# Optimization experiments

Hardware: AMD Instinct MI355X
Metric: run time of the kernel (lower is better)

The kernel has to match this reference:

```python
import jax, jax.numpy as jnp
import numpy as np

N = 100000
E = 1600000
IN_FEATS = 512
N_CLASSES = 40
H1, D1 = 8, 8
H2, D2 = 1, N_CLASSES


def gat_conv(x, src, dst, W, al, ar, b, H, D):
    # x: [N, F] -> h: [N, H, D]
    n = x.shape[0]
    h = (x @ W).reshape(n, H, D)
    el = (h * al[None]).sum(-1)  # [N, H]
    er = (h * ar[None]).sum(-1)  # [N, H]
    e = jax.nn.leaky_relu(el[src] + er[dst], 0.2)  # [E, H]
    # segment softmax over destination neighborhoods
    emax = jax.ops.segment_max(e, dst, num_segments=n)  # [N, H]
    ee = jnp.exp(e - emax[dst])
    denom = jax.ops.segment_sum(ee, dst, num_segments=n)  # [N, H]
    a = ee / (denom[dst] + 1e-9)  # [E, H]
    m = h[src] * a[:, :, None]  # [E, H, D]
    out = jax.ops.segment_sum(m, dst, num_segments=n)  # [N, H, D]
    return out + b.reshape(1, H, D)


def setup_inputs() -> dict:
    key = jax.random.key(0)
    ks = jax.random.split(key, 12)
    g1 = 1.0 / np.sqrt(IN_FEATS)
    g2 = 1.0 / np.sqrt(H1 * D1)
    return {
        "x": jax.random.normal(ks[0], (N, IN_FEATS), jnp.float32),
        "src": jax.random.randint(ks[1], (E,), 0, N, jnp.int32),
        "dst": jax.random.randint(ks[2], (E,), 0, N, jnp.int32),
        "W1": jax.random.normal(ks[3], (IN_FEATS, H1 * D1), jnp.float32) * g1,
        "al1": jax.random.normal(ks[4], (H1, D1), jnp.float32) * 0.1,
        "ar1": jax.random.normal(ks[5], (H1, D1), jnp.float32) * 0.1,
        "b1": jnp.zeros((H1 * D1,), jnp.float32),
        "W2": jax.random.normal(ks[6], (H1 * D1, H2 * D2), jnp.float32) * g2,
        "al2": jax.random.normal(ks[7], (H2, D2), jnp.float32) * 0.1,
        "ar2": jax.random.normal(ks[8], (H2, D2), jnp.float32) * 0.1,
        "b2": jnp.zeros((H2 * D2,), jnp.float32),
    }


def reference(x, src, dst, W1, al1, ar1, b1, W2, al2, ar2, b2):
    h = gat_conv(x, src, dst, W1, al1, ar1, b1, H1, D1)  # [N, 8, 8]
    h = jax.nn.elu(h.reshape(N, H1 * D1))  # [N, 64]
    h = gat_conv(h, src, dst, W2, al2, ar2, b2, H2, D2).mean(axis=1)  # [N, n_classes]
    return jax.nn.log_softmax(h, axis=1)
```

## Files before the change

### kernel.cpp

```cpp
#include <hip/hip_runtime.h>
#include <hip/hip_bf16.h>
#include <math.h>

#define NCLS 40
#define PWG 256
#define BSH 9
#define NBMAX 512
#define SRCB 23
#define CSRCAP 14336

typedef __attribute__((ext_vector_type(8))) short bf16x8;
typedef __attribute__((ext_vector_type(4))) float f32x4;

__device__ inline float bf2f(ushort u) {
    unsigned v = ((unsigned)u) << 16;
    float f;
    __builtin_memcpy(&f, &v, 4);
    return f;
}
__device__ inline ushort f2bf(float f) {
    unsigned v;
    __builtin_memcpy(&v, &f, 4);
    unsigned r = (v + 0x7FFFu + ((v >> 16) & 1u)) >> 16;
    return (ushort)r;
}

__global__ __launch_bounds__(256) void conv_prep_kernel(
    const float* __restrict__ W1, ushort* __restrict__ W1t,
    const float* __restrict__ W2, const float* __restrict__ al2,
    const float* __restrict__ ar2, float* __restrict__ wal2,
    float* __restrict__ war2)
{
    if (blockIdx.x < 128) {
        int id = blockIdx.x * 256 + threadIdx.x;
        int k = id >> 6, c = id & 63;
        W1t[c * 512 + k] = f2bf(W1[k * 64 + c]);
    } else {
        int k = threadIdx.x;
        if (k < 64) {
            float a = 0.f, b = 0.f;
            for (int c = 0; c < NCLS; c++) {
                float w = W2[k * NCLS + c];
                a += w * al2[c];
                b += w * ar2[c];
            }
            wal2[k] = a;
            war2[k] = b;
        }
    }
}

__global__ __launch_bounds__(256) void gemm1_mfma_kernel(
    const float* __restrict__ x, const ushort* __restrict__ W1t,
    const float* __restrict__ al1, const float* __restrict__ ar1,
    ushort* __restrict__ h1b, float* __restrict__ el1,
    float* __restrict__ er1, int Nn)
{
    __shared__ ushort As[64 * 72];
    __shared__ ushort Bs[64 * 72];
    const int t = threadIdx.x;
    const int lane = t & 63, w = t >> 6;
    const int tile = blockIdx.x * 64;

    f32x4 acc[4] = {};

    const int sr = t >> 2;
    const int sk = (t & 3) * 16;
    const int arow = tile + sr;
    const bool rowok = arow < Nn;
    const float* xrow = x + (size_t)arow * 512;
    const ushort* wrow = W1t + (size_t)sr * 512;

    const int r = lane & 15, g = lane >> 4;

    float4 f0 = make_float4(0.f, 0.f, 0.f, 0.f), f1 = f0, f2 = f0, f3 = f0;
    bf16x8 bv0, bv1;
    if (rowok) {
        f0 = *(const float4*)(xrow + sk);
        f1 = *(const float4*)(xrow + sk + 4);
        f2 = *(const float4*)(xrow + sk + 8);
        f3 = *(const float4*)(xrow + sk + 12);
    }
    bv0 = *(const bf16x8*)(wrow + sk);
    bv1 = *(const bf16x8*)(wrow + sk + 8);

    for (int k0 = 0; k0 < 512; k0 += 64) {
        bf16x8 av0, av1;
        av0[0] = (short)f2bf(f0.x); av0[1] = (short)f2bf(f0.y);
        av0[2] = (short)f2bf(f0.z); av0[3] = (short)f2bf(f0.w);
        av0[4] = (short)f2bf(f1.x); av0[5] = (short)f2bf(f1.y);
        av0[6] = (short)f2bf(f1.z); av0[7] = (short)f2bf(f1.w);
        av1[0] = (short)f2bf(f2.x); av1[1] = (short)f2bf(f2.y);
        av1[2] = (short)f2bf(f2.z); av1[3] = (short)f2bf(f2.w);
        av1[4] = (short)f2bf(f3.x); av1[5] = (short)f2bf(f3.y);
        av1[6] = (short)f2bf(f3.z); av1[7] = (short)f2bf(f3.w);
        *(bf16x8*)&As[sr * 72 + sk] = av0;
        *(bf16x8*)&As[sr * 72 + sk + 8] = av1;
        *(bf16x8*)&Bs[sr * 72 + sk] = bv0;
        *(bf16x8*)&Bs[sr * 72 + sk + 8] = bv1;
        __syncthreads();

        int k1 = k0 + 64;
        if (k1 < 512) {
            if (rowok) {
                f0 = *(const float4*)(xrow + k1 + sk);
                f1 = *(const float4*)(xrow + k1 + sk + 4);
                f2 = *(const float4*)(xrow + k1 + sk + 8);
                f3 = *(const float4*)(xrow + k1 + sk + 12);
            }
            bv0 = *(const bf16x8*)(wrow + k1 + sk);
            bv1 = *(const bf16x8*)(wrow + k1 + sk + 8);
        }

        bf16x8 af0 = *(const bf16x8*)&As[(w * 16 + r) * 72 + g * 8];
        bf16x8 af1 = *(const bf16x8*)&As[(w * 16 + r) * 72 + 32 + g * 8];
#pragma unroll
        for (int cb = 0; cb < 4; cb++) {
            bf16x8 bf0 = *(const bf16x8*)&Bs[(cb * 16 + r) * 72 + g * 8];
            acc[cb] = __builtin_amdgcn_mfma_f32_16x16x32_bf16(af0, bf0, acc[cb], 0, 0, 0);
        }
#pragma unroll
        for (int cb = 0; cb < 4; cb++) {
            bf16x8 bf1 = *(const bf16x8*)&Bs[(cb * 16 + r) * 72 + 32 + g * 8];
            acc[cb] = __builtin_amdgcn_mfma_f32_16x16x32_bf16(af1, bf1, acc[cb], 0, 0, 0);
        }
        __syncthreads();
    }

    float alv[4], arv[4];
#pragma unroll
    for (int cb = 0; cb < 4; cb++) {
        alv[cb] = al1[cb * 16 + r];
        arv[cb] = ar1[cb * 16 + r];
    }
#pragma unroll
    for (int v = 0; v < 4; v++) {
        int row = tile + w * 16 + g * 4 + v;
        bool ok = row < Nn;
#pragma unroll
        for (int cb = 0; cb < 4; cb++) {
            if (ok) h1b[(size_t)row * 64 + cb * 16 + r] = f2bf(acc[cb][v]);
            float pel = acc[cb][v] * alv[cb];
            float per = acc[cb][v] * arv[cb];
            pel += __shfl_xor(pel, 1); per += __shfl_xor(per, 1);
            pel += __shfl_xor(pel, 2); per += __shfl_xor(per, 2);
            pel += __shfl_xor(pel, 4); per += __shfl_xor(per, 4);
            if (ok && (r & 7) == 0) {
                int head = cb * 2 + (r >> 3);
                el1[row * 8 + head] = pel;
                er1[row * 8 + head] = per;
            }
        }
    }
}

__global__ __launch_bounds__(256) void hist_kernel(const int* __restrict__ dst,
                                                   int* __restrict__ hist,
                                                   int Ee, int chunk, int NB)
{
    __shared__ int lh[NBMAX];
    const int wg = blockIdx.x, tid = threadIdx.x;
    for (int i = tid; i < NB; i += 256) lh[i] = 0;
    __syncthreads();
    const int beg = wg * chunk;
    const int endv = min(Ee, beg + chunk);
    for (int i = beg + tid; i < endv; i += 256) atomicAdd(&lh[dst[i] >> BSH], 1);
    __syncthreads();
    for (int b = tid; b < NB; b += 256) hist[b * PWG + wg] = lh[b];
}

__global__ __launch_bounds__(256) void scanA_kernel(int* __restrict__ hist,
                                                    int* __restrict__ bucketTot)
{
    __shared__ int s[256];
    const int b = blockIdx.x, tid = threadIdx.x;
    int v = hist[b * PWG + tid];
    s[tid] = v;
    __syncthreads();
#pragma unroll
    for (int o = 1; o < 256; o <<= 1) {
        int t = (tid >= o) ? s[tid - o] : 0;
        __syncthreads();
        s[tid] += t;
        __syncthreads();
    }
    hist[b * PWG + tid] = s[tid] - v;
    if (tid == 255) bucketTot[b] = s[255];
}

__global__ __launch_bounds__(256) void scanB_kernel(const int* __restrict__ bucketTot,
                                                    int* __restrict__ bucketBase,
                                                    int NB, int Ee)
{
    __shared__ int s[256];
    const int tid = threadIdx.x;
    int v = (tid < NB) ? bucketTot[tid] : 0;
    s[tid] = v;
    __syncthreads();
#pragma unroll
    for (int o = 1; o < 256; o <<= 1) {
        int t = (tid >= o) ? s[tid - o] : 0;
        __syncthreads();
        s[tid] += t;
        __syncthreads();
    }
    if (tid < NB) bucketBase[tid] = s[tid] - v;
    if (tid == 0) bucketBase[NB] = Ee;
}

__global__ __launch_bounds__(256) void partition_kernel(const int* __restrict__ src,
                                                        const int* __restrict__ dst,
                                                        const int* __restrict__ hist,
                                                        const int* __restrict__ bucketBase,
                                                        unsigned* __restrict__ ebuf,
                                                        int Ee, int chunk, int NB)
{
    __shared__ int cur[NBMAX];
    const int wg = blockIdx.x, tid = threadIdx.x;
    for (int b = tid; b < NB; b += 256) cur[b] = hist[b * PWG + wg] + bucketBase[b];
    __syncthreads();
    const int beg = wg * chunk;
    const int endv = min(Ee, beg + chunk);
    for (int i = beg + tid; i < endv; i += 256) {
        int d = dst[i];
        int p = atomicAdd(&cur[d >> BSH], 1);
        ebuf[p] = ((unsigned)(d & ((1 << BSH) - 1)) << SRCB) | (unsigned)src[i];
    }
}

__global__ __launch_bounds__(512) void bucket_csr_kernel(const unsigned* __restrict__ ebuf,
                                                         const int* __restrict__ bucketBase,
                                                         int* __restrict__ row_start,
                                                         int* __restrict__ perm_src,
                                                         int Nn, int Ee, int NB)
{
    __shared__ unsigned stage[CSRCAP];
    __shared__ int cnt[512];
    __shared__ int s[512];
    __shared__ int cur[512];
    const int b = blockIdx.x, tid = threadIdx.x;
    const int base = b << BSH;
    const int bb = bucketBase[b], be = bucketBase[b + 1];
    const int m = be - bb;

    cnt[tid] = 0;
    __syncthreads();
    for (int idx = tid; idx < m; idx += 512) {
        unsigned pk = ebuf[bb + idx];
        if (idx < CSRCAP) stage[idx] = pk;
        atomicAdd(&cnt[pk >> SRCB], 1);
    }
    __syncthreads();
    int v = cnt[tid];
    s[tid] = v;
    __syncthreads();
#pragma unroll
    for (int o = 1; o < 512; o <<= 1) {
        int t = (tid >= o) ? s[tid - o] : 0;
        __syncthreads();
        s[tid] += t;
        __syncthreads();
    }
    const int off = bb + s[tid] - v;
    const int node = base + tid;
    if (node < Nn) row_start[node] = off;
    cur[tid] = off;
    __syncthreads();
    for (int idx = tid; idx < m; idx += 512) {
        unsigned pk = (idx < CSRCAP) ? stage[idx] : ebuf[bb + idx];
        int p = atomicAdd(&cur[pk >> SRCB], 1);
        perm_src[p] = (int)(pk & ((1u << SRCB) - 1u));
    }
    if (b == NB - 1 && tid == 0) row_start[Nn] = Ee;
}

__global__ __launch_bounds__(256) void agg1_kernel(
    const ushort* __restrict__ h1b, const float* __restrict__ el1,
    const float* __restrict__ er1, const int* __restrict__ row_start,
    const int* __restrict__ perm_src, const float* __restrict__ b1,
    ushort* __restrict__ hmidb, int Nn)
{
    int wid = (blockIdx.x * blockDim.x + threadIdx.x) >> 6;
    int lane = threadIdx.x & 63;
    if (wid >= Nn) return;
    const int h = lane >> 3;
    const int beg = row_start[wid], end = row_start[wid + 1];
    const float er = er1[wid * 8 + h];

    float acc = 0.f, denom = 0.f;
    for (int i0 = beg; i0 < end; i0 += 64) {
        int cnt = min(end - i0, 64);
        int pv = (i0 + lane < end) ? perm_src[i0 + lane] : 0;
        int j = 0;
        for (; j + 8 <= cnt; j += 8) {
            int ss[8];
#pragma unroll
            for (int u = 0; u < 8; u++) ss[u] = __shfl(pv, j + u);
            float ev[8];
            ushort rv[8];
#pragma unroll
            for (int u = 0; u < 8; u++) ev[u] = el1[ss[u] * 8 + h];
#pragma unroll
            for (int u = 0; u < 8; u++) rv[u] = h1b[(size_t)ss[u] * 64 + lane];
#pragma unroll
            for (int u = 0; u < 8; u++) {
                float e = ev[u] + er;
                e = (e >= 0.f) ? e : 0.2f * e;
                float w = __expf(fminf(e, 80.f));
                denom += w;
                acc += bf2f(rv[u]) * w;
            }
        }
        for (; j + 4 <= cnt; j += 4) {
            int ss[4];
#pragma unroll
            for (int u = 0; u < 4; u++) ss[u] = __shfl(pv, j + u);
            float ev[4];
            ushort rv[4];
#pragma unroll
            for (int u = 0; u < 4; u++) ev[u] = el1[ss[u] * 8 + h];
#pragma unroll
            for (int u = 0; u < 4; u++) rv[u] = h1b[(size_t)ss[u] * 64 + lane];
#pragma unroll
            for (int u = 0; u < 4; u++) {
                float e = ev[u] + er;
                e = (e >= 0.f) ? e : 0.2f * e;
                float w = __expf(fminf(e, 80.f));
                denom += w;
                acc += bf2f(rv[u]) * w;
            }
        }
        for (; j < cnt; j++) {
            int sI = __shfl(pv, j);
            float e = el1[sI * 8 + h] + er;
            e = (e >= 0.f) ? e : 0.2f * e;
            float w = __expf(fminf(e, 80.f));
            denom += w;
            acc += bf2f(h1b[(size_t)sI * 64 + lane]) * w;
        }
    }
    float v = acc / (denom + 1e-9f) + b1[lane];
    v = (v > 0.f) ? v : expm1f(v);
    hmidb[(size_t)wid * 64 + lane] = f2bf(v);
}

__global__ __launch_bounds__(256) void gemm2_kernel(
    const ushort* __restrict__ hmidb, const float* __restrict__ W2,
    const float* __restrict__ wal2, const float* __restrict__ war2,
    ushort* __restrict__ h2b, float* __restrict__ el2, float* __restrict__ er2,
    int Nn)
{
    __shared__ float w2s[64 * NCLS];
    __shared__ float wals[64], wars[64];
    for (int i = threadIdx.x; i < 64 * NCLS; i += blockDim.x) w2s[i] = W2[i];
    if (threadIdx.x < 64) {
        wals[threadIdx.x] = wal2[threadIdx.x];
        wars[threadIdx.x] = war2[threadIdx.x];
    }
    __syncthreads();
    int n = blockIdx.x * blockDim.x + threadIdx.x;
    if (n >= Nn) return;

    float out[NCLS];
#pragma unroll
    for (int c = 0; c < NCLS; c++) out[c] = 0.f;
    float accel = 0.f, accer = 0.f;

#pragma unroll 4
    for (int k4 = 0; k4 < 16; k4++) {
        ushort4 u = *(const ushort4*)&hmidb[(size_t)n * 64 + k4 * 4];
        float h0 = bf2f(u.x), h1 = bf2f(u.y), h2 = bf2f(u.z), h3 = bf2f(u.w);
        accel += h0 * wals[k4 * 4] + h1 * wals[k4 * 4 + 1] + h2 * wals[k4 * 4 + 2] + h3 * wals[k4 * 4 + 3];
        accer += h0 * wars[k4 * 4] + h1 * wars[k4 * 4 + 1] + h2 * wars[k4 * 4 + 2] + h3 * wars[k4 * 4 + 3];
#pragma unroll
        for (int c = 0; c < NCLS; c++) {
            out[c] += h0 * w2s[(k4 * 4 + 0) * NCLS + c] + h1 * w2s[(k4 * 4 + 1) * NCLS + c] +
                      h2 * w2s[(k4 * 4 + 2) * NCLS + c] + h3 * w2s[(k4 * 4 + 3) * NCLS + c];
        }
    }
    el2[n] = accel;
    er2[n] = accer;
#pragma unroll
    for (int c = 0; c < NCLS; c++) h2b[(size_t)n * NCLS + c] = f2bf(out[c]);
}

__global__ __launch_bounds__(256) void agg2_kernel(
    const ushort* __restrict__ h2b, const float* __restrict__ el2,
    const float* __restrict__ er2, const int* __restrict__ row_start,
    const int* __restrict__ perm_src, const float* __restrict__ b2,
    float* __restrict__ out, int Nn)
{
    int wid = (blockIdx.x * blockDim.x + threadIdx.x) >> 6;
    int lane = threadIdx.x & 63;
    if (wid >= Nn) return;
    const int beg = row_start[wid], end = row_start[wid + 1];
    const float er = er2[wid];
    const bool act = lane < NCLS;
    const int cl = act ? lane : 0;

    float acc = 0.f, denom = 0.f;
    for (int i0 = beg; i0 < end; i0 += 64) {
        int cnt = min(end - i0, 64);
        int pv = (i0 + lane < end) ? perm_src[i0 + lane] : 0;
        int j = 0;
        for (; j + 8 <= cnt; j += 8) {
            int ss[8];
#pragma unroll
            for (int u = 0; u < 8; u++) ss[u] = __shfl(pv, j + u);
            float ev[8];
            ushort rv[8];
#pragma unroll
            for (int u = 0; u < 8; u++) ev[u] = el2[ss[u]];
#pragma unroll
            for (int u = 0; u < 8; u++) rv[u] = h2b[(size_t)ss[u] * NCLS + cl];
#pragma unroll
            for (int u = 0; u < 8; u++) {
                float e = ev[u] + er;
                e = (e >= 0.f) ? e : 0.2f * e;
                float w = __expf(fminf(e, 80.f));
                denom += w;
                acc += bf2f(rv[u]) * w;
            }
        }
        for (; j + 4 <= cnt; j += 4) {
            int ss[4];
#pragma unroll
            for (int u = 0; u < 4; u++) ss[u] = __shfl(pv, j + u);
            float ev[4];
            ushort rv[4];
#pragma unroll
            for (int u = 0; u < 4; u++) ev[u] = el2[ss[u]];
#pragma unroll
            for (int u = 0; u < 4; u++) rv[u] = h2b[(size_t)ss[u] * NCLS + cl];
#pragma unroll
            for (int u = 0; u < 4; u++) {
                float e = ev[u] + er;
                e = (e >= 0.f) ? e : 0.2f * e;
                float w = __expf(fminf(e, 80.f));
                denom += w;
                acc += bf2f(rv[u]) * w;
            }
        }
        for (; j < cnt; j++) {
            int sI = __shfl(pv, j);
            float e = el2[sI] + er;
            e = (e >= 0.f) ? e : 0.2f * e;
            float w = __expf(fminf(e, 80.f));
            denom += w;
            acc += bf2f(h2b[(size_t)sI * NCLS + cl]) * w;
        }
    }
    float v = act ? (acc / (denom + 1e-9f) + b2[lane]) : -1e30f;

    float mx = v;
#pragma unroll
    for (int o = 1; o < 64; o <<= 1) mx = fmaxf(mx, __shfl_xor(mx, o));
    float sx = act ? __expf(v - mx) : 0.f;
#pragma unroll
    for (int o = 1; o < 64; o <<= 1) sx += __shfl_xor(sx, o);
    if (act) out[(size_t)wid * NCLS + lane] = v - mx - __logf(sx);
}

extern "C" void kernel_launch(void* const* d_in, const int* in_sizes, int n_in,
                              void* d_out, int out_size, void* d_ws, size_t ws_size,
                              hipStream_t stream)
{
    const float* x   = (const float*)d_in[0];
    const int*   src = (const int*)d_in[1];
    const int*   dst = (const int*)d_in[2];
    const float* W1  = (const float*)d_in[3];
    const float* al1 = (const float*)d_in[4];
    const float* ar1 = (const float*)d_in[5];
    const float* b1  = (const float*)d_in[6];
    const float* W2  = (const float*)d_in[7];
    const float* al2 = (const float*)d_in[8];
    const float* ar2 = (const float*)d_in[9];
    const float* b2  = (const float*)d_in[10];
    float* out = (float*)d_out;

    const int Nn = in_sizes[0] / 512;
    const int Ee = in_sizes[1];
    const int NB = (Nn + (1 << BSH) - 1) >> BSH;
    const int chunk = (Ee + PWG - 1) / PWG;

    char* wsb = (char*)d_ws;
    size_t off = 0;
    auto alloc = [&](size_t bytes) -> void* {
        off = (off + 15) & ~(size_t)15;
        void* p = wsb + off;
        off += bytes;
        return p;
    };
    ushort* h1b   = (ushort*)alloc((size_t)Nn * 64 * 2);
    ushort* hmidb = (ushort*)alloc((size_t)Nn * 64 * 2);
    ushort* h2b   = (ushort*)alloc((size_t)Nn * NCLS * 2);
    ushort* W1t   = (ushort*)alloc(64 * 512 * 2);
    float* el1  = (float*)alloc((size_t)Nn * 8 * 4);
    float* er1  = (float*)alloc((size_t)Nn * 8 * 4);
    float* el2  = (float*)alloc((size_t)Nn * 4);
    float* er2  = (float*)alloc((size_t)Nn * 4);
    float* wal2 = (float*)alloc(64 * 4);
    float* war2 = (float*)alloc(64 * 4);
    int* row_start  = (int*)alloc((size_t)(Nn + 1) * 4);
    int* hist       = (int*)alloc((size_t)NB * PWG * 4);
    int* bucketTot  = (int*)alloc((size_t)NB * 4);
    int* bucketBase = (int*)alloc((size_t)(NB + 1) * 4);
    int* perm_src   = (int*)alloc((size_t)Ee * 4);
    unsigned* ebuf  = (unsigned*)alloc((size_t)Ee * 4);

    hist_kernel<<<PWG, 256, 0, stream>>>(dst, hist, Ee, chunk, NB);
    scanA_kernel<<<NB, 256, 0, stream>>>(hist, bucketTot);
    scanB_kernel<<<1, 256, 0, stream>>>(bucketTot, bucketBase, NB, Ee);
    partition_kernel<<<PWG, 256, 0, stream>>>(src, dst, hist, bucketBase, ebuf, Ee, chunk, NB);
    bucket_csr_kernel<<<NB, 512, 0, stream>>>(ebuf, bucketBase, row_start, perm_src, Nn, Ee, NB);

    conv_prep_kernel<<<129, 256, 0, stream>>>(W1, W1t, W2, al2, ar2, wal2, war2);
    gemm1_mfma_kernel<<<(Nn + 63) / 64, 256, 0, stream>>>(x, W1t, al1, ar1, h1b, el1, er1, Nn);
    agg1_kernel<<<(Nn + 3) / 4, 256, 0, stream>>>(h1b, el1, er1, row_start, perm_src, b1, hmidb, Nn);

    gemm2_kernel<<<(Nn + 255) / 256, 256, 0, stream>>>(hmidb, W2, wal2, war2, h2b, el2, er2, Nn);
    agg2_kernel<<<(Nn + 3) / 4, 256, 0, stream>>>(h2b, el2, er2, row_start, perm_src, b2, out, Nn);
}
```

Before: 264.4 us.

## Fuse layer-2 GEMM into agg1 and pack el2/er2 into padded h2 rows

Computes the el1 attention logits on the fly in agg1 from the gathered bf16 h1 row with a shuffle reduction, so the el1 array is no longer gathered. gemm2 is folded into the end of agg1: each wave multiplies its ELU output by W2 held in shared memory and writes h2 to a 64-wide row with el2/er2 stored in the padding. This removes the hmidb round trip, the gemm2 launch, and the separate el/er gathers in agg2. In exchange agg1 does more shuffles per edge and a per-block W2 load into shared memory, and h2 rows grow from 40 to 64 elements.

```diff
diff --git a/kernel.cpp b/kernel.cpp
--- a/kernel.cpp
+++ b/kernel.cpp
@@ -3,6 +3,7 @@
 #include <math.h>
 
 #define NCLS 40
+#define H2S 64
 #define PWG 256
 #define BSH 9
 #define NBMAX 512
@@ -52,8 +53,7 @@
 
 __global__ __launch_bounds__(256) void gemm1_mfma_kernel(
     const float* __restrict__ x, const ushort* __restrict__ W1t,
-    const float* __restrict__ al1, const float* __restrict__ ar1,
-    ushort* __restrict__ h1b, float* __restrict__ el1,
+    const float* __restrict__ ar1, ushort* __restrict__ h1b,
     float* __restrict__ er1, int Nn)
 {
     __shared__ ushort As[64 * 72];
@@ -127,12 +127,9 @@
         __syncthreads();
     }
 
-    float alv[4], arv[4];
-#pragma unroll
-    for (int cb = 0; cb < 4; cb++) {
-        alv[cb] = al1[cb * 16 + r];
-        arv[cb] = ar1[cb * 16 + r];
-    }
+    float arv4[4];
+#pragma unroll
+    for (int cb = 0; cb < 4; cb++) arv4[cb] = ar1[cb * 16 + r];
 #pragma unroll
     for (int v = 0; v < 4; v++) {
         int row = tile + w * 16 + g * 4 + v;
@@ -140,15 +137,12 @@
 #pragma unroll
         for (int cb = 0; cb < 4; cb++) {
             if (ok) h1b[(size_t)row * 64 + cb * 16 + r] = f2bf(acc[cb][v]);
-            float pel = acc[cb][v] * alv[cb];
-            float per = acc[cb][v] * arv[cb];
-            pel += __shfl_xor(pel, 1); per += __shfl_xor(per, 1);
-            pel += __shfl_xor(pel, 2); per += __shfl_xor(per, 2);
-            pel += __shfl_xor(pel, 4); per += __shfl_xor(per, 4);
+            float per = acc[cb][v] * arv4[cb];
+            per += __shfl_xor(per, 1);
+            per += __shfl_xor(per, 2);
+            per += __shfl_xor(per, 4);
             if (ok && (r & 7) == 0) {
-                int head = cb * 2 + (r >> 3);
-                el1[row * 8 + head] = pel;
-                er1[row * 8 + head] = per;
+                er1[row * 8 + cb * 2 + (r >> 3)] = per;
             }
         }
     }
@@ -274,18 +268,31 @@
     if (b == NB - 1 && tid == 0) row_start[Nn] = Ee;
 }
 
-__global__ __launch_bounds__(256) void agg1_kernel(
-    const ushort* __restrict__ h1b, const float* __restrict__ el1,
+__global__ __launch_bounds__(256) void agg1_fused_kernel(
+    const ushort* __restrict__ h1b, const float* __restrict__ al1,
     const float* __restrict__ er1, const int* __restrict__ row_start,
     const int* __restrict__ perm_src, const float* __restrict__ b1,
-    ushort* __restrict__ hmidb, int Nn)
-{
-    int wid = (blockIdx.x * blockDim.x + threadIdx.x) >> 6;
-    int lane = threadIdx.x & 63;
+    const float* __restrict__ W2, const float* __restrict__ wal2,
+    const float* __restrict__ war2, ushort* __restrict__ h2b, int Nn)
+{
+    __shared__ float w2s[64 * NCLS];
+    __shared__ float wals[64], wars[64];
+    __shared__ float hm[4][64];
+    for (int i = threadIdx.x; i < 64 * NCLS; i += 256) w2s[i] = W2[i];
+    if (threadIdx.x < 64) {
+        wals[threadIdx.x] = wal2[threadIdx.x];
+        wars[threadIdx.x] = war2[threadIdx.x];
+    }
+    __syncthreads();
+
+    const int wid = (blockIdx.x * blockDim.x + threadIdx.x) >> 6;
+    const int lane = threadIdx.x & 63;
+    const int w = threadIdx.x >> 6;
     if (wid >= Nn) return;
     const int h = lane >> 3;
     const int beg = row_start[wid], end = row_start[wid + 1];
     const float er = er1[wid * 8 + h];
+    const float alv = al1[lane];
 
     float acc = 0.f, denom = 0.f;
     for (int i0 = beg; i0 < end; i0 += 64) {
@@ -294,99 +301,84 @@
         int j = 0;
         for (; j + 8 <= cnt; j += 8) {
             int ss[8];
+            ushort rv[8];
 #pragma unroll
             for (int u = 0; u < 8; u++) ss[u] = __shfl(pv, j + u);
-            float ev[8];
-            ushort rv[8];
-#pragma unroll
-            for (int u = 0; u < 8; u++) ev[u] = el1[ss[u] * 8 + h];
 #pragma unroll
             for (int u = 0; u < 8; u++) rv[u] = h1b[(size_t)ss[u] * 64 + lane];
 #pragma unroll
             for (int u = 0; u < 8; u++) {
-                float e = ev[u] + er;
+                float f = bf2f(rv[u]);
+                float p = f * alv;
+                p += __shfl_xor(p, 1);
+                p += __shfl_xor(p, 2);
+                p += __shfl_xor(p, 4);
+                float e = p + er;
                 e = (e >= 0.f) ? e : 0.2f * e;
-                float w = __expf(fminf(e, 80.f));
-                denom += w;
-                acc += bf2f(rv[u]) * w;
+                float wt = __expf(fminf(e, 80.f));
+                denom += wt;
+                acc += f * wt;
             }
         }
         for (; j + 4 <= cnt; j += 4) {
             int ss[4];
+            ushort rv[4];
 #pragma unroll
             for (int u = 0; u < 4; u++) ss[u] = __shfl(pv, j + u);
-            float ev[4];
-            ushort rv[4];
-#pragma unroll
-            for (int u = 0; u < 4; u++) ev[u] = el1[ss[u] * 8 + h];
 #pragma unroll
             for (int u = 0; u < 4; u++) rv[u] = h1b[(size_t)ss[u] * 64 + lane];
 #pragma unroll
             for (int u = 0; u < 4; u++) {
-                float e = ev[u] + er;
+                float f = bf2f(rv[u]);
+                float p = f * alv;
+                p += __shfl_xor(p, 1);
+                p += __shfl_xor(p, 2);
+                p += __shfl_xor(p, 4);
+                float e = p + er;
                 e = (e >= 0.f) ? e : 0.2f * e;
-                float w = __expf(fminf(e, 80.f));
-                denom += w;
-                acc += bf2f(rv[u]) * w;
+                float wt = __expf(fminf(e, 80.f));
+                denom += wt;
+                acc += f * wt;
             }
         }
         for (; j < cnt; j++) {
             int sI = __shfl(pv, j);
-            float e = el1[sI * 8 + h] + er;
+            float f = bf2f(h1b[(size_t)sI * 64 + lane]);
+            float p = f * alv;
+            p += __shfl_xor(p, 1);
+            p += __shfl_xor(p, 2);
+            p += __shfl_xor(p, 4);
+            float e = p + er;
             e = (e >= 0.f) ? e : 0.2f * e;
-            float w = __expf(fminf(e, 80.f));
-            denom += w;
-            acc += bf2f(h1b[(size_t)sI * 64 + lane]) * w;
+            float wt = __expf(fminf(e, 80.f));
+            denom += wt;
+            acc += f * wt;
         }
     }
     float v = acc / (denom + 1e-9f) + b1[lane];
     v = (v > 0.f) ? v : expm1f(v);
-    hmidb[(size_t)wid * 64 + lane] = f2bf(v);
-}
-
-__global__ __launch_bounds__(256) void gemm2_kernel(
-    const ushort* __restrict__ hmidb, const float* __restrict__ W2,
-    const float* __restrict__ wal2, const float* __restrict__ war2,
-    ushort* __restrict__ h2b, float* __restrict__ el2, float* __restrict__ er2,
-    int Nn)
-{
-    __shared__ float w2s[64 * NCLS];
-    __shared__ float wals[64], wars[64];
-    for (int i = threadIdx.x; i < 64 * NCLS; i += blockDim.x) w2s[i] = W2[i];
-    if (threadIdx.x < 64) {
-        wals[threadIdx.x] = wal2[threadIdx.x];
-        wars[threadIdx.x] = war2[threadIdx.x];
-    }
-    __syncthreads();
-    int n = blockIdx.x * blockDim.x + threadIdx.x;
-    if (n >= Nn) return;
-
-    float out[NCLS];
-#pragma unroll
-    for (int c = 0; c < NCLS; c++) out[c] = 0.f;
-    float accel = 0.f, accer = 0.f;
-
-#pragma unroll 4
-    for (int k4 = 0; k4 < 16; k4++) {
-        ushort4 u = *(const ushort4*)&hmidb[(size_t)n * 64 + k4 * 4];
-        float h0 = bf2f(u.x), h1 = bf2f(u.y), h2 = bf2f(u.z), h3 = bf2f(u.w);
-        accel += h0 * wals[k4 * 4] + h1 * wals[k4 * 4 + 1] + h2 * wals[k4 * 4 + 2] + h3 * wals[k4 * 4 + 3];
-        accer += h0 * wars[k4 * 4] + h1 * wars[k4 * 4 + 1] + h2 * wars[k4 * 4 + 2] + h3 * wars[k4 * 4 + 3];
-#pragma unroll
-        for (int c = 0; c < NCLS; c++) {
-            out[c] += h0 * w2s[(k4 * 4 + 0) * NCLS + c] + h1 * w2s[(k4 * 4 + 1) * NCLS + c] +
-                      h2 * w2s[(k4 * 4 + 2) * NCLS + c] + h3 * w2s[(k4 * 4 + 3) * NCLS + c];
-        }
-    }
-    el2[n] = accel;
-    er2[n] = accer;
-#pragma unroll
-    for (int c = 0; c < NCLS; c++) h2b[(size_t)n * NCLS + c] = f2bf(out[c]);
+
+    hm[w][lane] = v;
+    float pe = v * wals[lane];
+    float pr = v * wars[lane];
+#pragma unroll
+    for (int o = 1; o < 64; o <<= 1) {
+        pe += __shfl_xor(pe, o);
+        pr += __shfl_xor(pr, o);
+    }
+    float outc = 0.f;
+    if (lane < NCLS) {
+#pragma unroll 8
+        for (int k = 0; k < 64; k++) outc += hm[w][k] * w2s[k * NCLS + lane];
+    }
+    ushort* row = h2b + (size_t)wid * H2S;
+    if (lane < NCLS) row[lane] = f2bf(outc);
+    if (lane == NCLS) ((float*)row)[20] = pe;
+    if (lane == NCLS + 1) ((float*)row)[21] = pr;
 }
 
 __global__ __launch_bounds__(256) void agg2_kernel(
-    const ushort* __restrict__ h2b, const float* __restrict__ el2,
-    const float* __restrict__ er2, const int* __restrict__ row_start,
+    const ushort* __restrict__ h2b, const int* __restrict__ row_start,
     const int* __restrict__ perm_src, const float* __restrict__ b2,
     float* __restrict__ out, int Nn)
 {
@@ -394,7 +386,7 @@
     int lane = threadIdx.x & 63;
     if (wid >= Nn) return;
     const int beg = row_start[wid], end = row_start[wid + 1];
-    const float er = er2[wid];
+    const float er = ((const float*)(h2b + (size_t)wid * H2S))[21];
     const bool act = lane < NCLS;
     const int cl = act ? lane : 0;
 
@@ -405,14 +397,16 @@
         int j = 0;
         for (; j + 8 <= cnt; j += 8) {
             int ss[8];
-#pragma unroll
-            for (int u = 0; u < 8; u++) ss[u] = __shfl(pv, j + u);
             float ev[8];
             ushort rv[8];
 #pragma unroll
-            for (int u = 0; u < 8; u++) ev[u] = el2[ss[u]];
-#pragma unroll
-            for (int u = 0; u < 8; u++) rv[u] = h2b[(size_t)ss[u] * NCLS + cl];
+            for (int u = 0; u < 8; u++) ss[u] = __shfl(pv, j + u);
+#pragma unroll
+            for (int u = 0; u < 8; u++) {
+                const ushort* rp = h2b + (size_t)ss[u] * H2S;
+                rv[u] = rp[cl];
+                ev[u] = ((const float*)rp)[20];
+            }
 #pragma unroll
             for (int u = 0; u < 8; u++) {
                 float e = ev[u] + er;
@@ -424,14 +418,16 @@
         }
         for (; j + 4 <= cnt; j += 4) {
             int ss[4];
-#pragma unroll
-            for (int u = 0; u < 4; u++) ss[u] = __shfl(pv, j + u);
             float ev[4];
             ushort rv[4];
 #pragma unroll
-            for (int u = 0; u < 4; u++) ev[u] = el2[ss[u]];
-#pragma unroll
-            for (int u = 0; u < 4; u++) rv[u] = h2b[(size_t)ss[u] * NCLS + cl];
+            for (int u = 0; u < 4; u++) ss[u] = __shfl(pv, j + u);
+#pragma unroll
+            for (int u = 0; u < 4; u++) {
+                const ushort* rp = h2b + (size_t)ss[u] * H2S;
+                rv[u] = rp[cl];
+                ev[u] = ((const float*)rp)[20];
+            }
 #pragma unroll
             for (int u = 0; u < 4; u++) {
                 float e = ev[u] + er;
@@ -443,11 +439,12 @@
         }
         for (; j < cnt; j++) {
             int sI = __shfl(pv, j);
-            float e = el2[sI] + er;
+            const ushort* rp = h2b + (size_t)sI * H2S;
+            float e = ((const float*)rp)[20] + er;
             e = (e >= 0.f) ? e : 0.2f * e;
             float w = __expf(fminf(e, 80.f));
             denom += w;
-            acc += bf2f(h2b[(size_t)sI * NCLS + cl]) * w;
+            acc += bf2f(rp[cl]) * w;
         }
     }
     float v = act ? (acc / (denom + 1e-9f) + b2[lane]) : -1e30f;
@@ -492,13 +489,9 @@
         return p;
     };
     ushort* h1b   = (ushort*)alloc((size_t)Nn * 64 * 2);
-    ushort* hmidb = (ushort*)alloc((size_t)Nn * 64 * 2);
-    ushort* h2b   = (ushort*)alloc((size_t)Nn * NCLS * 2);
+    ushort* h2b   = (ushort*)alloc((size_t)Nn * H2S * 2);
     ushort* W1t   = (ushort*)alloc(64 * 512 * 2);
-    float* el1  = (float*)alloc((size_t)Nn * 8 * 4);
     float* er1  = (float*)alloc((size_t)Nn * 8 * 4);
-    float* el2  = (float*)alloc((size_t)Nn * 4);
-    float* er2  = (float*)alloc((size_t)Nn * 4);
     float* wal2 = (float*)alloc(64 * 4);
     float* war2 = (float*)alloc(64 * 4);
     int* row_start  = (int*)alloc((size_t)(Nn + 1) * 4);
@@ -515,9 +508,9 @@
     bucket_csr_kernel<<<NB, 512, 0, stream>>>(ebuf, bucketBase, row_start, perm_src, Nn, Ee, NB);
 
     conv_prep_kernel<<<129, 256, 0, stream>>>(W1, W1t, W2, al2, ar2, wal2, war2);
-    gemm1_mfma_kernel<<<(Nn + 63) / 64, 256, 0, stream>>>(x, W1t, al1, ar1, h1b, el1, er1, Nn);
-    agg1_kernel<<<(Nn + 3) / 4, 256, 0, stream>>>(h1b, el1, er1, row_start, perm_src, b1, hmidb, Nn);
-
-    gemm2_kernel<<<(Nn + 255) / 256, 256, 0, stream>>>(hmidb, W2, wal2, war2, h2b, el2, er2, Nn);
-    agg2_kernel<<<(Nn + 3) / 4, 256, 0, stream>>>(h2b, el2, er2, row_start, perm_src, b2, out, Nn);
-}
+    gemm1_mfma_kernel<<<(Nn + 63) / 64, 256, 0, stream>>>(x, W1t, ar1, h1b, er1, Nn);
+    agg1_fused_kernel<<<(Nn + 3) / 4, 256, 0, stream>>>(h1b, al1, er1, row_start, perm_src,
+                                                        b1, W2, wal2, war2, h2b, Nn);
+
+    agg2_kernel<<<(Nn + 3) / 4, 256, 0, stream>>>(h2b, row_start, perm_src, b2, out, Nn);
+}
```

After: 301.4 us. 14.0% more time.

## Pack layer-2 features with attention logits and vectorize layer-1 aggregation

Applied to the files above, without the earlier changes.

Layer-1 aggregation is restructured so each wave processes 4 edges at once: 16-lane groups each handle one edge with 4-wide bf16 vector loads, then partial sums are reduced across groups by shuffles. Layer 2 stores h2 rows padded to 64 bf16 with el2/er2 embedded in the padding, so one gathered 128-byte row supplies both features and logit, removing separate scattered el2 loads. This costs extra cross-lane reductions and a larger h2 buffer. The layer-1 path also drops the exp clamp.

```diff
diff --git a/kernel.cpp b/kernel.cpp
--- a/kernel.cpp
+++ b/kernel.cpp
@@ -3,6 +3,7 @@
 #include <math.h>
 
 #define NCLS 40
+#define H2S 64
 #define PWG 256
 #define BSH 9
 #define NBMAX 512
@@ -280,12 +281,117 @@
     const int* __restrict__ perm_src, const float* __restrict__ b1,
     ushort* __restrict__ hmidb, int Nn)
 {
+    const int wid = (blockIdx.x * blockDim.x + threadIdx.x) >> 6;
+    const int lane = threadIdx.x & 63;
+    if (wid >= Nn) return;
+    const int g = lane >> 4;
+    const int q = lane & 15;
+    const int h = q >> 1;
+    const int beg = row_start[wid], end = row_start[wid + 1];
+    const float er = er1[wid * 8 + h];
+
+    float a0 = 0.f, a1 = 0.f, a2 = 0.f, a3 = 0.f, denom = 0.f;
+    for (int i0 = beg; i0 < end; i0 += 64) {
+        const int cnt = min(end - i0, 64);
+        int pv = (i0 + lane < end) ? perm_src[i0 + lane] : 0;
+        for (int j = 0; j < cnt; j += 8) {
+            const int e0 = j + g, e1 = j + 4 + g;
+            const int s0 = __shfl(pv, min(e0, cnt - 1));
+            const int s1 = __shfl(pv, min(e1, cnt - 1));
+            ushort4 r0 = *(const ushort4*)&h1b[(size_t)s0 * 64 + q * 4];
+            ushort4 r1 = *(const ushort4*)&h1b[(size_t)s1 * 64 + q * 4];
+            float x0 = el1[s0 * 8 + h];
+            float x1 = el1[s1 * 8 + h];
+            float e = x0 + er;
+            e = (e >= 0.f) ? e : 0.2f * e;
+            float w0 = (e0 < cnt) ? __expf(e) : 0.f;
+            e = x1 + er;
+            e = (e >= 0.f) ? e : 0.2f * e;
+            float w1 = (e1 < cnt) ? __expf(e) : 0.f;
+            denom += w0 + w1;
+            a0 += bf2f(r0.x) * w0 + bf2f(r1.x) * w1;
+            a1 += bf2f(r0.y) * w0 + bf2f(r1.y) * w1;
+            a2 += bf2f(r0.z) * w0 + bf2f(r1.z) * w1;
+            a3 += bf2f(r0.w) * w0 + bf2f(r1.w) * w1;
+        }
+    }
+    denom += __shfl_xor(denom, 16); denom += __shfl_xor(denom, 32);
+    a0 += __shfl_xor(a0, 16); a0 += __shfl_xor(a0, 32);
+    a1 += __shfl_xor(a1, 16); a1 += __shfl_xor(a1, 32);
+    a2 += __shfl_xor(a2, 16); a2 += __shfl_xor(a2, 32);
+    a3 += __shfl_xor(a3, 16); a3 += __shfl_xor(a3, 32);
+    if (g == 0) {
+        const float4 bv = *(const float4*)&b1[q * 4];
+        const float inv = 1.f / (denom + 1e-9f);
+        float v0 = a0 * inv + bv.x;
+        float v1 = a1 * inv + bv.y;
+        float v2 = a2 * inv + bv.z;
+        float v3 = a3 * inv + bv.w;
+        v0 = (v0 > 0.f) ? v0 : expm1f(v0);
+        v1 = (v1 > 0.f) ? v1 : expm1f(v1);
+        v2 = (v2 > 0.f) ? v2 : expm1f(v2);
+        v3 = (v3 > 0.f) ? v3 : expm1f(v3);
+        ushort4 o;
+        o.x = f2bf(v0); o.y = f2bf(v1); o.z = f2bf(v2); o.w = f2bf(v3);
+        *(ushort4*)&hmidb[(size_t)wid * 64 + q * 4] = o;
+    }
+}
+
+__global__ __launch_bounds__(256) void gemm2_kernel(
+    const ushort* __restrict__ hmidb, const float* __restrict__ W2,
+    const float* __restrict__ wal2, const float* __restrict__ war2,
+    ushort* __restrict__ h2b, int Nn)
+{
+    __shared__ float w2s[64 * NCLS];
+    __shared__ float wals[64], wars[64];
+    for (int i = threadIdx.x; i < 64 * NCLS; i += blockDim.x) w2s[i] = W2[i];
+    if (threadIdx.x < 64) {
+        wals[threadIdx.x] = wal2[threadIdx.x];
+        wars[threadIdx.x] = war2[threadIdx.x];
+    }
+    __syncthreads();
+    int n = blockIdx.x * blockDim.x + threadIdx.x;
+    if (n >= Nn) return;
+
+    float out[NCLS];
+#pragma unroll
+    for (int c = 0; c < NCLS; c++) out[c] = 0.f;
+    float accel = 0.f, accer = 0.f;
+
+#pragma unroll 4
+    for (int k4 = 0; k4 < 16; k4++) {
+        ushort4 u = *(const ushort4*)&hmidb[(size_t)n * 64 + k4 * 4];
+        float h0 = bf2f(u.x), h1 = bf2f(u.y), h2 = bf2f(u.z), h3 = bf2f(u.w);
+        accel += h0 * wals[k4 * 4] + h1 * wals[k4 * 4 + 1] + h2 * wals[k4 * 4 + 2] + h3 * wals[k4 * 4 + 3];
+        accer += h0 * wars[k4 * 4] + h1 * wars[k4 * 4 + 1] + h2 * wars[k4 * 4 + 2] + h3 * wars[k4 * 4 + 3];
+#pragma unroll
+        for (int c = 0; c < NCLS; c++) {
+            out[c] += h0 * w2s[(k4 * 4 + 0) * NCLS + c] + h1 * w2s[(k4 * 4 + 1) * NCLS + c] +
+                      h2 * w2s[(k4 * 4 + 2) * NCLS + c] + h3 * w2s[(k4 * 4 + 3) * NCLS + c];
+        }
+    }
+    ushort* row = h2b + (size_t)n * H2S;
+#pragma unroll
+    for (int c = 0; c < NCLS; c += 2) {
+        unsigned pk = (unsigned)f2bf(out[c]) | ((unsigned)f2bf(out[c + 1]) << 16);
+        *(unsigned*)&row[c] = pk;
+    }
+    ((float*)row)[20] = accel;
+    ((float*)row)[21] = accer;
+}
+
+__global__ __launch_bounds__(256) void agg2_kernel(
+    const ushort* __restrict__ h2b, const int* __restrict__ row_start,
+    const int* __restrict__ perm_src, const float* __restrict__ b2,
+    float* __restrict__ out, int Nn)
+{
     int wid = (blockIdx.x * blockDim.x + threadIdx.x) >> 6;
     int lane = threadIdx.x & 63;
     if (wid >= Nn) return;
-    const int h = lane >> 3;
     const int beg = row_start[wid], end = row_start[wid + 1];
-    const float er = er1[wid * 8 + h];
+    const float er = ((const float*)(h2b + (size_t)wid * H2S))[21];
+    const bool act = lane < NCLS;
+    const int cl = act ? lane : 0;
 
     float acc = 0.f, denom = 0.f;
     for (int i0 = beg; i0 < end; i0 += 64) {
@@ -294,14 +400,16 @@
         int j = 0;
         for (; j + 8 <= cnt; j += 8) {
             int ss[8];
-#pragma unroll
-            for (int u = 0; u < 8; u++) ss[u] = __shfl(pv, j + u);
             float ev[8];
             ushort rv[8];
 #pragma unroll
-            for (int u = 0; u < 8; u++) ev[u] = el1[ss[u] * 8 + h];
-#pragma unroll
-            for (int u = 0; u < 8; u++) rv[u] = h1b[(size_t)ss[u] * 64 + lane];
+            for (int u = 0; u < 8; u++) ss[u] = __shfl(pv, j + u);
+#pragma unroll
+            for (int u = 0; u < 8; u++) {
+                const ushort* rp = h2b + (size_t)ss[u] * H2S;
+                rv[u] = rp[cl];
+                ev[u] = ((const float*)rp)[20];
+            }
 #pragma unroll
             for (int u = 0; u < 8; u++) {
                 float e = ev[u] + er;
@@ -313,14 +421,16 @@
         }
         for (; j + 4 <= cnt; j += 4) {
             int ss[4];
-#pragma unroll
-            for (int u = 0; u < 4; u++) ss[u] = __shfl(pv, j + u);
             float ev[4];
             ushort rv[4];
 #pragma unroll
-            for (int u = 0; u < 4; u++) ev[u] = el1[ss[u] * 8 + h];
-#pragma unroll
-            for (int u = 0; u < 4; u++) rv[u] = h1b[(size_t)ss[u] * 64 + lane];
+            for (int u = 0; u < 4; u++) ss[u] = __shfl(pv, j + u);
+#pragma unroll
+            for (int u = 0; u < 4; u++) {
+                const ushort* rp = h2b + (size_t)ss[u] * H2S;
+                rv[u] = rp[cl];
+                ev[u] = ((const float*)rp)[20];
+            }
 #pragma unroll
             for (int u = 0; u < 4; u++) {
                 float e = ev[u] + er;
@@ -332,122 +442,12 @@
         }
         for (; j < cnt; j++) {
             int sI = __shfl(pv, j);
-            float e = el1[sI * 8 + h] + er;
+            const ushort* rp = h2b + (size_t)sI * H2S;
+            float e = ((const float*)rp)[20] + er;
             e = (e >= 0.f) ? e : 0.2f * e;
             float w = __expf(fminf(e, 80.f));
             denom += w;
-            acc += bf2f(h1b[(size_t)sI * 64 + lane]) * w;
-        }
-    }
-    float v = acc / (denom + 1e-9f) + b1[lane];
-    v = (v > 0.f) ? v : expm1f(v);
-    hmidb[(size_t)wid * 64 + lane] = f2bf(v);
-}
-
-__global__ __launch_bounds__(256) void gemm2_kernel(
-    const ushort* __restrict__ hmidb, const float* __restrict__ W2,
-    const float* __restrict__ wal2, const float* __restrict__ war2,
-    ushort* __restrict__ h2b, float* __restrict__ el2, float* __restrict__ er2,
-    int Nn)
-{
-    __shared__ float w2s[64 * NCLS];
-    __shared__ float wals[64], wars[64];
-    for (int i = threadIdx.x; i < 64 * NCLS; i += blockDim.x) w2s[i] = W2[i];
-    if (threadIdx.x < 64) {
-        wals[threadIdx.x] = wal2[threadIdx.x];
-        wars[threadIdx.x] = war2[threadIdx.x];
-    }
-    __syncthreads();
-    int n = blockIdx.x * blockDim.x + threadIdx.x;
-    if (n >= Nn) return;
-
-    float out[NCLS];
-#pragma unroll
-    for (int c = 0; c < NCLS; c++) out[c] = 0.f;
-    float accel = 0.f, accer = 0.f;
-
-#pragma unroll 4
-    for (int k4 = 0; k4 < 16; k4++) {
-        ushort4 u = *(const ushort4*)&hmidb[(size_t)n * 64 + k4 * 4];
-        float h0 = bf2f(u.x), h1 = bf2f(u.y), h2 = bf2f(u.z), h3 = bf2f(u.w);
-        accel += h0 * wals[k4 * 4] + h1 * wals[k4 * 4 + 1] + h2 * wals[k4 * 4 + 2] + h3 * wals[k4 * 4 + 3];
-        accer += h0 * wars[k4 * 4] + h1 * wars[k4 * 4 + 1] + h2 * wars[k4 * 4 + 2] + h3 * wars[k4 * 4 + 3];
-#pragma unroll
-        for (int c = 0; c < NCLS; c++) {
-            out[c] += h0 * w2s[(k4 * 4 + 0) * NCLS + c] + h1 * w2s[(k4 * 4 + 1) * NCLS + c] +
-                      h2 * w2s[(k4 * 4 + 2) * NCLS + c] + h3 * w2s[(k4 * 4 + 3) * NCLS + c];
-        }
-    }
-    el2[n] = accel;
-    er2[n] = accer;
-#pragma unroll
-    for (int c = 0; c < NCLS; c++) h2b[(size_t)n * NCLS + c] = f2bf(out[c]);
-}
-
-__global__ __launch_bounds__(256) void agg2_kernel(
-    const ushort* __restrict__ h2b, const float* __restrict__ el2,
-    const float* __restrict__ er2, const int* __restrict__ row_start,
-    const int* __restrict__ perm_src, const float* __restrict__ b2,
-    float* __restrict__ out, int Nn)
-{
-    int wid = (blockIdx.x * blockDim.x + threadIdx.x) >> 6;
-    int lane = threadIdx.x & 63;
-    if (wid >= Nn) return;
-    const int beg = row_start[wid], end = row_start[wid + 1];
-    const float er = er2[wid];
-    const bool act = lane < NCLS;
-    const int cl = act ? lane : 0;
-
-    float acc = 0.f, denom = 0.f;
-    for (int i0 = beg; i0 < end; i0 += 64) {
-        int cnt = min(end - i0, 64);
-        int pv = (i0 + lane < end) ? perm_src[i0 + lane] : 0;
-        int j = 0;
-        for (; j + 8 <= cnt; j += 8) {
-            int ss[8];
-#pragma unroll
-            for (int u = 0; u < 8; u++) ss[u] = __shfl(pv, j + u);
-            float ev[8];
-            ushort rv[8];
-#pragma unroll
-            for (int u = 0; u < 8; u++) ev[u] = el2[ss[u]];
-#pragma unroll
-            for (int u = 0; u < 8; u++) rv[u] = h2b[(size_t)ss[u] * NCLS + cl];
-#pragma unroll
-            for (int u = 0; u < 8; u++) {
-                float e = ev[u] + er;
-                e = (e >= 0.f) ? e : 0.2f * e;
-                float w = __expf(fminf(e, 80.f));
-                denom += w;
-                acc += bf2f(rv[u]) * w;
-            }
-        }
-        for (; j + 4 <= cnt; j += 4) {
-            int ss[4];
-#pragma unroll
-            for (int u = 0; u < 4; u++) ss[u] = __shfl(pv, j + u);
-            float ev[4];
-            ushort rv[4];
-#pragma unroll
-            for (int u = 0; u < 4; u++) ev[u] = el2[ss[u]];
-#pragma unroll
-            for (int u = 0; u < 4; u++) rv[u] = h2b[(size_t)ss[u] * NCLS + cl];
-#pragma unroll
-            for (int u = 0; u < 4; u++) {
-                float e = ev[u] + er;
-                e = (e >= 0.f) ? e : 0.2f * e;
-                float w = __expf(fminf(e, 80.f));
-                denom += w;
-                acc += bf2f(rv[u]) * w;
-            }
-        }
-        for (; j < cnt; j++) {
-            int sI = __shfl(pv, j);
-            float e = el2[sI] + er;
-            e = (e >= 0.f) ? e : 0.2f * e;
-            float w = __expf(fminf(e, 80.f));
-            denom += w;
-            acc += bf2f(h2b[(size_t)sI * NCLS + cl]) * w;
+            acc += bf2f(rp[cl]) * w;
         }
     }
     float v = act ? (acc / (denom + 1e-9f) + b2[lane]) : -1e30f;
@@ -493,12 +493,10 @@
     };
     ushort* h1b   = (ushort*)alloc((size_t)Nn * 64 * 2);
     ushort* hmidb = (ushort*)alloc((size_t)Nn * 64 * 2);
-    ushort* h2b   = (ushort*)alloc((size_t)Nn * NCLS * 2);
+    ushort* h2b   = (ushort*)alloc((size_t)Nn * H2S * 2);
     ushort* W1t   = (ushort*)alloc(64 * 512 * 2);
     float* el1  = (float*)alloc((size_t)Nn * 8 * 4);
     float* er1  = (float*)alloc((size_t)Nn * 8 * 4);
-    float* el2  = (float*)alloc((size_t)Nn * 4);
-    float* er2  = (float*)alloc((size_t)Nn * 4);
     float* wal2 = (float*)alloc(64 * 4);
     float* war2 = (float*)alloc(64 * 4);
     int* row_start  = (int*)alloc((size_t)(Nn + 1) * 4);
@@ -518,6 +516,6 @@
     gemm1_mfma_kernel<<<(Nn + 63) / 64, 256, 0, stream>>>(x, W1t, al1, ar1, h1b, el1, er1, Nn);
     agg1_kernel<<<(Nn + 3) / 4, 256, 0, stream>>>(h1b, el1, er1, row_start, perm_src, b1, hmidb, Nn);
 
-    gemm2_kernel<<<(Nn + 255) / 256, 256, 0, stream>>>(hmidb, W2, wal2, war2, h2b, el2, er2, Nn);
-    agg2_kernel<<<(Nn + 3) / 4, 256, 0, stream>>>(h2b, el2, er2, row_start, perm_src, b2, out, Nn);
-}
+    gemm2_kernel<<<(Nn + 255) / 256, 256, 0, stream>>>(hmidb, W2, wal2, war2, h2b, Nn);
+    agg2_kernel<<<(Nn + 3) / 4, 256, 0, stream>>>(h2b, row_start, perm_src, b2, out, Nn);
+}
```

Result: faster. 258.6 us (-2.2%).
